# Optimization experiments

Hardware: AMD Instinct MI355X
Metric: run time of the kernel (lower is better)

Reference implementation:

```python
import jax, jax.numpy as jnp
import numpy as np

NEG_INF = -1e9  # stands in for the eye(W)*sys.maxsize self-mask on the row axis


def setup_inputs() -> dict:
    key = jax.random.key(0)
    ks = jax.random.split(key, 8)
    B, C, S = 8, 512, 128
    C8 = C // 8
    sc = 0.02
    x = jax.random.normal(ks[0], (B, C, S, S), dtype=jnp.float32)
    Wq = jax.random.normal(ks[1], (C8, C), dtype=jnp.float32) * sc
    bq = jnp.zeros((C8,), dtype=jnp.float32)
    Wk = jax.random.normal(ks[2], (C8, C), dtype=jnp.float32) * sc
    bk = jnp.zeros((C8,), dtype=jnp.float32)
    Wv = jax.random.normal(ks[3], (C, C), dtype=jnp.float32) * sc
    bv = jnp.zeros((C,), dtype=jnp.float32)
    gamma = jnp.ones((1,), dtype=jnp.float32) * 0.5  # source inits to 0; nonzero so path is exercised
    return {"x": x, "Wq": Wq, "bq": bq, "Wk": Wk, "bk": bk, "Wv": Wv, "bv": bv, "gamma": gamma}


def reference(x, Wq, bq, Wk, bk, Wv, bv, gamma):
    # x: (B, C, W, H) with W == H == S (required by the eye-mask view in the source)
    B, C, S, _ = x.shape
    # 1x1 convs = per-pixel linear projections
    q = jnp.einsum('oc,bcwh->bowh', Wq, x) + bq[None, :, None, None]  # (B,C8,S,S)
    k = jnp.einsum('oc,bcwh->bowh', Wk, x) + bk[None, :, None, None]
    v = jnp.einsum('oc,bcwh->bowh', Wv, x) + bv[None, :, None, None]  # (B,C,S,S)

    # column ('h'-fixed) attention along W, self position masked out
    e_col = jnp.einsum('bcwh,bcuh->bwhu', q, k)  # (B,W,H,W)
    self_mask = jnp.eye(S, dtype=bool)  # w == u
    e_col = jnp.where(self_mask[None, :, None, :], NEG_INF, e_col)
    # row ('w'-fixed) attention along H
    e_row = jnp.einsum('bcwh,bcwu->bwhu', q, k)  # (B,W,H,H)

    att = jax.nn.softmax(jnp.concatenate([e_col, e_row], axis=-1), axis=-1)  # (B,W,H,2S)
    a_col = att[..., :S]   # weights over w'
    a_row = att[..., S:]   # weights over h'

    out = (jnp.einsum('bwhu,bcuh->bcwh', a_col, v)
           + jnp.einsum('bwhu,bcwu->bcwh', a_row, v))  # (B,C,S,S)
    return gamma[0] * out + x
```

## Files before the change

### kernel.cpp

```cpp
#include <hip/hip_runtime.h>
#include <hip/hip_bf16.h>


#define S 128
#define SS 16384
#define C 512
#define C8 64
#define NEG_BIG -1000000000.0f

using short8 = __attribute__((ext_vector_type(8))) short;
using f32x4  = __attribute__((ext_vector_type(4))) float;

#define GPTR(p) ((const __attribute__((address_space(1))) void*)(p))
#define LPTR(p) ((__attribute__((address_space(3))) void*)(p))

#define PR(r) ((((r) & 7) << 4) | ((r) >> 3))

__device__ __forceinline__ unsigned short f2b(float f){
  union { float f; unsigned u; } v; v.f = f;
  unsigned r = (v.u + 0x7fffu + ((v.u >> 16) & 1u)) >> 16;
  return (unsigned short)r;
}
__device__ __forceinline__ float b2f(unsigned short h){
  union { unsigned u; float f; } v; v.u = ((unsigned)h) << 16;
  return v.f;
}

__device__ __forceinline__ void stage_tile64(unsigned short* dst,
    const unsigned short* src, size_t rstride, int tid){
  #pragma unroll
  for (int p = 0; p < 4; ++p){
    int gi = p * 256 + tid;
    int row = gi >> 3, cc = gi & 7;
    int kc = (cc ^ (row & 7)) * 8;
    __builtin_amdgcn_global_load_lds(GPTR(src + (size_t)row * rstride + kc),
                                     LPTR((char*)dst + gi * 16), 16, 0, 0);
  }
}

__global__ __launch_bounds__(256) void k_pack_w(
    const float* __restrict__ Wq, const float* __restrict__ Wk,
    const float* __restrict__ Wv, unsigned short* __restrict__ wall){
  int i = blockIdx.x * 256 + threadIdx.x;
  if (i >= 640 * C) return;
  int co = i >> 9, ci = i & (C - 1);
  float v;
  if (co < 64)        v = Wq[co * C + ci];
  else if (co < 128)  v = Wk[(co - 64) * C + ci];
  else                v = Wv[(co - 128) * C + ci];
  wall[i] = f2b(v);
}

__global__ __launch_bounds__(256) void k_xp(
    const float* __restrict__ x, unsigned short* __restrict__ xp){
  __shared__ unsigned short T[128 * 130] __attribute__((aligned(16)));
  int blk = blockIdx.x;
  int ct = blk & 3; int bw = blk >> 2;
  int w = bw & 127; int b = bw >> 7;
  int tid = threadIdx.x;
  int ci0 = ct * 128;
  const float* xb = x + ((size_t)(b * C + ci0) * S + w) * S;
  #pragma unroll
  for (int p = 0; p < 16; ++p){
    int idx = p * 256 + tid;
    int cc = idx >> 5;
    int h4 = (idx & 31) * 4;
    float4 v = *(const float4*)(xb + (size_t)cc * SS + h4);
    unsigned* d = (unsigned*)&T[PR(cc) * 130 + h4];
    d[0] = (unsigned)f2b(v.x) | ((unsigned)f2b(v.y) << 16);
    d[1] = (unsigned)f2b(v.z) | ((unsigned)f2b(v.w) << 16);
  }
  __syncthreads();
  unsigned short* xpb = xp + (size_t)(b * S + w) * S * C + ci0;
  #pragma unroll
  for (int p = 0; p < 8; ++p){
    int idx = p * 256 + tid;
    int h  = idx >> 4;
    int ch = (idx & 15) * 8;
    unsigned short tmp[8] __attribute__((aligned(16)));
    #pragma unroll
    for (int j = 0; j < 8; ++j) tmp[j] = T[PR(ch + j) * 130 + h];
    *(uint4*)(xpb + (size_t)h * C + ch) = *(uint4*)tmp;
  }
}

__global__ __launch_bounds__(256) void k_qkv(
    const unsigned short* __restrict__ xp, const unsigned short* __restrict__ wall,
    const float* __restrict__ bq, const float* __restrict__ bk,
    const float* __restrict__ bv,
    unsigned short* __restrict__ qp, unsigned short* __restrict__ kp,
    unsigned short* __restrict__ vb){
  __shared__ unsigned short sm[32768] __attribute__((aligned(16)));
  unsigned short* Dl = sm;
  int blk = blockIdx.x;
  int pxsub = blk & 7; int t = blk >> 3;
  int cot = t % 5; int pxg = t / 5;
  int pxt = pxg * 8 + pxsub;
  int w = pxt & 127, b = pxt >> 7;
  int tid = threadIdx.x, lane = tid & 63, wid = tid >> 6;
  int qd = lane >> 4, ln = lane & 15;
  const unsigned short* asrc0 = wall + (size_t)cot * 128 * C;
  const unsigned short* bsrc0 = xp + (size_t)pxt * 128 * C;
  f32x4 acc[4][4];
  #pragma unroll
  for (int i = 0; i < 4; ++i)
    #pragma unroll
    for (int j = 0; j < 4; ++j) acc[i][j] = (f32x4){0.f, 0.f, 0.f, 0.f};

  stage_tile64(sm,        asrc0, C, tid);
  stage_tile64(sm + 8192, bsrc0, C, tid);
  __syncthreads();

  for (int kw = 0; kw < 8; ++kw){
    unsigned short* Acur = sm + (kw & 1) * 16384;
    unsigned short* Bcur = Acur + 8192;
    if (kw < 7){
      unsigned short* Anxt = sm + ((kw + 1) & 1) * 16384;
      stage_tile64(Anxt,        asrc0 + (kw + 1) * 64, C, tid);
      stage_tile64(Anxt + 8192, bsrc0 + (kw + 1) * 64, C, tid);
    }
    __builtin_amdgcn_s_setprio(1);
    #pragma unroll
    for (int ks = 0; ks < 2; ++ks){
      int ch8 = (((ks * 4 + qd) ^ (ln & 7)) * 8);
      short8 af[4], bfr[4];
      #pragma unroll
      for (int i = 0; i < 4; ++i)
        af[i] = *(const short8*)&Acur[(((wid & 1) * 4 + i) * 16 + ln) * 64 + ch8];
      #pragma unroll
      for (int j = 0; j < 4; ++j)
        bfr[j] = *(const short8*)&Bcur[(((wid >> 1) * 4 + j) * 16 + ln) * 64 + ch8];
      #pragma unroll
      for (int i = 0; i < 4; ++i)
        #pragma unroll
        for (int j = 0; j < 4; ++j)
          acc[i][j] = __builtin_amdgcn_mfma_f32_16x16x32_bf16(af[i], bfr[j], acc[i][j], 0, 0, 0);
    }
    __builtin_amdgcn_s_setprio(0);
    __syncthreads();
  }
  float bias_[4][4];
  #pragma unroll
  for (int i = 0; i < 4; ++i){
    int co_l0 = ((wid & 1) * 4 + i) * 16 + qd * 4;
    #pragma unroll
    for (int r = 0; r < 4; ++r){
      int co_l = co_l0 + r;
      bias_[i][r] = (cot == 0) ? (co_l < 64 ? bq[co_l] : bk[co_l - 64])
                               : bv[(cot - 1) * 128 + co_l];
    }
  }
  #pragma unroll
  for (int i = 0; i < 4; ++i){
    int co_l0 = ((wid & 1) * 4 + i) * 16 + qd * 4;
    #pragma unroll
    for (int j = 0; j < 4; ++j){
      int pxl = ((wid >> 1) * 4 + j) * 16 + ln;
      #pragma unroll
      for (int r = 0; r < 4; ++r)
        Dl[(co_l0 + r) * 136 + pxl] = f2b(acc[i][j][r] + bias_[i][r]);
    }
  }
  __syncthreads();
  if (cot == 0){
    unsigned short* qb = qp + (size_t)(b * S + w) * S * C8;
    unsigned short* kb = kp + (size_t)(b * S + w) * S * C8;
    #pragma unroll
    for (int p = 0; p < 4; ++p){
      int idx = p * 256 + tid;
      int cch = idx & 7, hh = idx >> 3;
      unsigned short tq[8] __attribute__((aligned(16)));
      unsigned short tk[8] __attribute__((aligned(16)));
      #pragma unroll
      for (int jj = 0; jj < 8; ++jj){
        tq[jj] = Dl[(cch * 8 + jj) * 136 + hh];
        tk[jj] = Dl[(64 + cch * 8 + jj) * 136 + hh];
      }
      *(uint4*)(qb + (size_t)hh * C8 + cch * 8) = *(uint4*)tq;
      *(uint4*)(kb + (size_t)hh * C8 + cch * 8) = *(uint4*)tk;
    }
  } else {
    unsigned short* vbb = vb + ((size_t)(b * C + (cot - 1) * 128) * S + w) * S;
    #pragma unroll
    for (int p = 0; p < 8; ++p){
      int idx = p * 256 + tid;
      int c_l = idx >> 4, hc = (idx & 15) * 8;
      uint4 v = *(const uint4*)&Dl[c_l * 136 + hc];
      *(uint4*)(vbb + (size_t)c_l * SS + hc) = v;
    }
  }
}

__global__ __launch_bounds__(256) void k_tv(
    const unsigned short* __restrict__ vb, unsigned short* __restrict__ vt){
  __shared__ unsigned short T[128 * 130] __attribute__((aligned(16)));
  int bc = blockIdx.x;
  const unsigned short* src = vb + (size_t)bc * SS;
  unsigned short* dst = vt + (size_t)bc * SS;
  int tid = threadIdx.x;
  #pragma unroll
  for (int p = 0; p < 8; ++p){
    int idx = p * 256 + tid;
    int wv = idx >> 4, ch = (idx & 15) * 8;
    uint4 v = *(const uint4*)(src + wv * S + ch);
    unsigned* d = (unsigned*)&T[PR(wv) * 130 + ch];
    d[0] = v.x; d[1] = v.y; d[2] = v.z; d[3] = v.w;
  }
  __syncthreads();
  #pragma unroll
  for (int p = 0; p < 8; ++p){
    int idx = p * 256 + tid;
    int h = idx >> 4, ch = (idx & 15) * 8;
    unsigned short tmp[8] __attribute__((aligned(16)));
    #pragma unroll
    for (int j = 0; j < 8; ++j) tmp[j] = T[PR(ch + j) * 130 + h];
    *(uint4*)(dst + h * S + ch) = *(uint4*)tmp;
  }
}

__global__ __launch_bounds__(256) void k_ecol(
    const unsigned short* __restrict__ qp, const unsigned short* __restrict__ kp,
    unsigned short* __restrict__ eca){
  __shared__ unsigned short Aq[128 * 72] __attribute__((aligned(16)));
  __shared__ unsigned short Bk[128 * 72] __attribute__((aligned(16)));
  int blk = blockIdx.x; int h = blk & 127, b = blk >> 7;
  int tid = threadIdx.x, lane = tid & 63, wid = tid >> 6;
  int qd = lane >> 4, ln = lane & 15;
  #pragma unroll
  for (int p = 0; p < 4; ++p){
    int idx = p * 256 + tid;
    int row = idx >> 3, ch = (idx & 7) * 8;
    *(uint4*)&Aq[row * 72 + ch] = *(const uint4*)(qp + ((size_t)(b * S + row) * S + h) * C8 + ch);
    *(uint4*)&Bk[row * 72 + ch] = *(const uint4*)(kp + ((size_t)(b * S + row) * S + h) * C8 + ch);
  }
  __syncthreads();
  f32x4 acc[4][4];
  #pragma unroll
  for (int i = 0; i < 4; ++i)
    #pragma unroll
    for (int j = 0; j < 4; ++j) acc[i][j] = (f32x4){0.f, 0.f, 0.f, 0.f};
  #pragma unroll
  for (int ks = 0; ks < 2; ++ks){
    int ko = ks * 32 + qd * 8;
    short8 af[4], bfr[4];
    #pragma unroll
    for (int i = 0; i < 4; ++i)
      af[i] = *(const short8*)&Aq[(((wid & 1) * 4 + i) * 16 + ln) * 72 + ko];
    #pragma unroll
    for (int j = 0; j < 4; ++j)
      bfr[j] = *(const short8*)&Bk[(((wid >> 1) * 4 + j) * 16 + ln) * 72 + ko];
    #pragma unroll
    for (int i = 0; i < 4; ++i)
      #pragma unroll
      for (int j = 0; j < 4; ++j)
        acc[i][j] = __builtin_amdgcn_mfma_f32_16x16x32_bf16(af[i], bfr[j], acc[i][j], 0, 0, 0);
  }
  #pragma unroll
  for (int i = 0; i < 4; ++i){
    int w0 = ((wid & 1) * 4 + i) * 16 + qd * 4;
    #pragma unroll
    for (int j = 0; j < 4; ++j){
      int ug = ((wid >> 1) * 4 + j) * 16 + ln;
      #pragma unroll
      for (int r = 0; r < 4; ++r){
        int wg = w0 + r;
        float val = acc[i][j][r];
        if (wg == ug) val = NEG_BIG;
        eca[((size_t)(b * S + wg) * S + h) * S + ug] = f2b(val);
      }
    }
  }
}

__global__ __launch_bounds__(256) void k_erow_sm_outrow(
    const unsigned short* __restrict__ qp, const unsigned short* __restrict__ kp,
    unsigned short* __restrict__ eca, unsigned short* vb){
  __shared__ char sm[71680] __attribute__((aligned(16)));
  unsigned short* Aq  = (unsigned short*)sm;
  unsigned short* Bk  = (unsigned short*)(sm + 18432);
  unsigned short* El  = (unsigned short*)sm;
  unsigned short* Av0 = (unsigned short*)(sm + 36864);
  unsigned short* Av1 = (unsigned short*)(sm + 53248);
  float* redm = (float*)(sm + 69632);
  float* reds = (float*)(sm + 70656);
  int blk = blockIdx.x; int w = blk & 127, b = blk >> 7;
  int tid = threadIdx.x, lane = tid & 63, wid = tid >> 6;
  int qd = lane >> 4, ln = lane & 15;
  size_t tb = (size_t)(b * S + w) * SS;
  const unsigned short* vsrc0 = vb + (size_t)(b * C) * SS + (size_t)w * S;

  {
    const unsigned short* qsrc = qp + (size_t)(b * S + w) * S * C8;
    const unsigned short* ksrc = kp + (size_t)(b * S + w) * S * C8;
    #pragma unroll
    for (int p = 0; p < 4; ++p){
      int idx = p * 256 + tid;
      int row = idx >> 3, ch = (idx & 7) * 8;
      *(uint4*)&Aq[row * 72 + ch] = *(const uint4*)(qsrc + row * C8 + ch);
      *(uint4*)&Bk[row * 72 + ch] = *(const uint4*)(ksrc + row * C8 + ch);
    }
  }
  stage_tile64(Av0, vsrc0, SS, tid);
  __syncthreads();
  f32x4 acc[4][4];
  #pragma unroll
  for (int i = 0; i < 4; ++i)
    #pragma unroll
    for (int j = 0; j < 4; ++j) acc[i][j] = (f32x4){0.f, 0.f, 0.f, 0.f};
  #pragma unroll
  for (int ks = 0; ks < 2; ++ks){
    int ko = ks * 32 + qd * 8;
    short8 af[4], bfr[4];
    #pragma unroll
    for (int i = 0; i < 4; ++i)
      af[i] = *(const short8*)&Aq[(((wid & 1) * 4 + i) * 16 + ln) * 72 + ko];
    #pragma unroll
    for (int j = 0; j < 4; ++j)
      bfr[j] = *(const short8*)&Bk[(((wid >> 1) * 4 + j) * 16 + ln) * 72 + ko];
    #pragma unroll
    for (int i = 0; i < 4; ++i)
      #pragma unroll
      for (int j = 0; j < 4; ++j)
        acc[i][j] = __builtin_amdgcn_mfma_f32_16x16x32_bf16(af[i], bfr[j], acc[i][j], 0, 0, 0);
  }
  __syncthreads();
  #pragma unroll
  for (int i = 0; i < 4; ++i){
    int h0 = ((wid & 1) * 4 + i) * 16 + qd * 4;
    #pragma unroll
    for (int j = 0; j < 4; ++j){
      int ul = ((wid >> 1) * 4 + j) * 16 + ln;
      #pragma unroll
      for (int r = 0; r < 4; ++r)
        El[(h0 + r) * 136 + ul] = f2b(acc[i][j][r]);
    }
  }
  __syncthreads();
  {
    int h = tid >> 1, half = tid & 1;
    const uint4* src4 = (half == 0) ? (const uint4*)(eca + tb + (size_t)h * S)
                                    : (const uint4*)&El[h * 136];
    float mx = -3.0e38f;
    #pragma unroll 4
    for (int u = 0; u < 16; ++u){
      uint4 v = src4[u];
      const unsigned short* e = (const unsigned short*)&v;
      #pragma unroll
      for (int jj = 0; jj < 8; ++jj) mx = fmaxf(mx, b2f(e[jj]));
    }
    redm[tid] = mx;
    __syncthreads();
    float m = fmaxf(mx, redm[tid ^ 1]);
    float s = 0.f;
    #pragma unroll 4
    for (int u = 0; u < 16; ++u){
      uint4 v = src4[u];
      const unsigned short* e = (const unsigned short*)&v;
      #pragma unroll
      for (int jj = 0; jj < 8; ++jj) s += __expf(b2f(e[jj]) - m);
    }
    reds[tid] = s;
    __syncthreads();
    float inv = 1.0f / (s + reds[tid ^ 1]);
    uint4* dst4 = (half == 0) ? (uint4*)(eca + tb + (size_t)h * S)
                              : (uint4*)&El[h * 136];
    #pragma unroll 4
    for (int u = 0; u < 16; ++u){
      uint4 v = src4[u];
      const unsigned short* e = (const unsigned short*)&v;
      unsigned short o[8] __attribute__((aligned(16)));
      #pragma unroll
      for (int jj = 0; jj < 8; ++jj) o[jj] = f2b(__expf(b2f(e[jj]) - m) * inv);
      dst4[u] = *(uint4*)o;
    }
  }
  __syncthreads();

  for (int s = 0; s < 8; ++s){
    int ct = s >> 1, kw = s & 1;
    unsigned short* Acur = (s & 1) ? Av1 : Av0;
    if (s < 7){
      int ct1 = (s + 1) >> 1, kw1 = (s + 1) & 1;
      stage_tile64((s & 1) ? Av0 : Av1,
                   vsrc0 + (size_t)(ct1 * 128) * SS + kw1 * 64, SS, tid);
    }
    if (kw == 0){
      #pragma unroll
      for (int i = 0; i < 4; ++i)
        #pragma unroll
        for (int j = 0; j < 4; ++j) acc[i][j] = (f32x4){0.f, 0.f, 0.f, 0.f};
    }
    __builtin_amdgcn_s_setprio(1);
    #pragma unroll
    for (int ks = 0; ks < 2; ++ks){
      int ch8 = (((ks * 4 + qd) ^ (ln & 7)) * 8);
      int ko = kw * 64 + ks * 32 + qd * 8;
      short8 af[4], bfr[4];
      #pragma unroll
      for (int i = 0; i < 4; ++i)
        af[i] = *(const short8*)&Acur[(((wid & 1) * 4 + i) * 16 + ln) * 64 + ch8];
      #pragma unroll
      for (int j = 0; j < 4; ++j)
        bfr[j] = *(const short8*)&El[(((wid >> 1) * 4 + j) * 16 + ln) * 136 + ko];
      #pragma unroll
      for (int i = 0; i < 4; ++i)
        #pragma unroll
        for (int j = 0; j < 4; ++j)
          acc[i][j] = __builtin_amdgcn_mfma_f32_16x16x32_bf16(af[i], bfr[j], acc[i][j], 0, 0, 0);
    }
    __builtin_amdgcn_s_setprio(0);
    if (kw == 1){
      #pragma unroll
      for (int i = 0; i < 4; ++i){
        int c0 = ((wid & 1) * 4 + i) * 16 + qd * 4;
        #pragma unroll
        for (int j = 0; j < 4; ++j){
          int hl = ((wid >> 1) * 4 + j) * 16 + ln;
          #pragma unroll
          for (int r = 0; r < 4; ++r){
            int cg = ct * 128 + c0 + r;
            vb[((size_t)(b * C + cg) * S + w) * S + hl] = f2b(acc[i][j][r]);
          }
        }
      }
    }
    __syncthreads();
  }
}

__global__ __launch_bounds__(256) void k_outcol(
    const unsigned short* __restrict__ vt, const unsigned short* __restrict__ eca,
    unsigned short* __restrict__ oct){
  __shared__ unsigned short Av[128 * 72] __attribute__((aligned(16)));
  __shared__ unsigned short Ba[128 * 72] __attribute__((aligned(16)));
  int blk = blockIdx.x;
  int ct = blk & 3; int bh = blk >> 2;
  int h = bh & 127, b = bh >> 7;
  int tid = threadIdx.x, lane = tid & 63, wid = tid >> 6;
  int qd = lane >> 4, ln = lane & 15;
  f32x4 acc[4][4];
  #pragma unroll
  for (int i = 0; i < 4; ++i)
    #pragma unroll
    for (int j = 0; j < 4; ++j) acc[i][j] = (f32x4){0.f, 0.f, 0.f, 0.f};
  for (int kw = 0; kw < 2; ++kw){
    __syncthreads();
    #pragma unroll
    for (int p = 0; p < 4; ++p){
      int idx = p * 256 + tid;
      int row = idx >> 3, ch = (idx & 7) * 8;
      *(uint4*)&Av[row * 72 + ch] =
        *(const uint4*)(vt + ((size_t)(b * C + ct * 128 + row) * S + h) * S + kw * 64 + ch);
      *(uint4*)&Ba[row * 72 + ch] =
        *(const uint4*)(eca + ((size_t)(b * S + row) * S + h) * S + kw * 64 + ch);
    }
    __syncthreads();
    #pragma unroll
    for (int ks = 0; ks < 2; ++ks){
      int ko = ks * 32 + qd * 8;
      short8 af[4], bfr[4];
      #pragma unroll
      for (int i = 0; i < 4; ++i)
        af[i] = *(const short8*)&Av[(((wid & 1) * 4 + i) * 16 + ln) * 72 + ko];
      #pragma unroll
      for (int j = 0; j < 4; ++j)
        bfr[j] = *(const short8*)&Ba[(((wid >> 1) * 4 + j) * 16 + ln) * 72 + ko];
      #pragma unroll
      for (int i = 0; i < 4; ++i)
        #pragma unroll
        for (int j = 0; j < 4; ++j)
          acc[i][j] = __builtin_amdgcn_mfma_f32_16x16x32_bf16(af[i], bfr[j], acc[i][j], 0, 0, 0);
    }
  }
  #pragma unroll
  for (int i = 0; i < 4; ++i){
    int c0 = ((wid & 1) * 4 + i) * 16 + qd * 4;
    #pragma unroll
    for (int j = 0; j < 4; ++j){
      int wl = ((wid >> 1) * 4 + j) * 16 + ln;
      #pragma unroll
      for (int r = 0; r < 4; ++r){
        int cg = ct * 128 + c0 + r;
        oct[((size_t)(b * S + h) * C + cg) * S + wl] = f2b(acc[i][j][r]);
      }
    }
  }
}

__global__ __launch_bounds__(256) void k_final(
    const unsigned short* __restrict__ oct, const unsigned short* __restrict__ orw,
    const float* __restrict__ x, const float* __restrict__ gamma,
    float* __restrict__ out){
  __shared__ unsigned short T[128 * 130] __attribute__((aligned(16)));
  int blk = blockIdx.x;
  int c = blk & 511, b = blk >> 9;
  int tid = threadIdx.x;
  float g = gamma[0];
  #pragma unroll
  for (int p = 0; p < 8; ++p){
    int idx = p * 256 + tid;
    int hh = idx >> 4, ch = (idx & 15) * 8;
    uint4 v = *(const uint4*)(oct + ((size_t)(b * S + hh) * C + c) * S + ch);
    unsigned* d = (unsigned*)&T[PR(hh) * 130 + ch];
    d[0] = v.x; d[1] = v.y; d[2] = v.z; d[3] = v.w;
  }
  __syncthreads();
  #pragma unroll
  for (int p = 0; p < 8; ++p){
    int idx = p * 256 + tid;
    int wv = idx >> 4, hch = (idx & 15) * 8;
    size_t o = ((size_t)(b * C + c) * S + wv) * S + hch;
    uint4 rv = *(const uint4*)(orw + o);
    const unsigned short* rr = (const unsigned short*)&rv;
    float4 x0 = *(const float4*)(x + o);
    float4 x1 = *(const float4*)(x + o + 4);
    float4 o0, o1;
    o0.x = g * (b2f(rr[0]) + b2f(T[PR(hch + 0) * 130 + wv])) + x0.x;
    o0.y = g * (b2f(rr[1]) + b2f(T[PR(hch + 1) * 130 + wv])) + x0.y;
    o0.z = g * (b2f(rr[2]) + b2f(T[PR(hch + 2) * 130 + wv])) + x0.z;
    o0.w = g * (b2f(rr[3]) + b2f(T[PR(hch + 3) * 130 + wv])) + x0.w;
    o1.x = g * (b2f(rr[4]) + b2f(T[PR(hch + 4) * 130 + wv])) + x1.x;
    o1.y = g * (b2f(rr[5]) + b2f(T[PR(hch + 5) * 130 + wv])) + x1.y;
    o1.z = g * (b2f(rr[6]) + b2f(T[PR(hch + 6) * 130 + wv])) + x1.z;
    o1.w = g * (b2f(rr[7]) + b2f(T[PR(hch + 7) * 130 + wv])) + x1.w;
    *(float4*)(out + o) = o0;
    *(float4*)(out + o + 4) = o1;
  }
}

extern "C" void kernel_launch(void* const* d_in, const int* in_sizes, int n_in,
                              void* d_out, int out_size, void* d_ws, size_t ws_size,
                              hipStream_t stream){
  const float* x     = (const float*)d_in[0];
  const float* Wq    = (const float*)d_in[1];
  const float* bq    = (const float*)d_in[2];
  const float* Wk    = (const float*)d_in[3];
  const float* bk    = (const float*)d_in[4];
  const float* Wv    = (const float*)d_in[5];
  const float* bv    = (const float*)d_in[6];
  const float* gamma = (const float*)d_in[7];
  float* out = (float*)d_out;
  char* ws = (char*)d_ws;

  const size_t OFF_WALL = 0;
  const size_t OFF_XP   = 1ull << 20;
  const size_t OFF_QP   = OFF_XP  + 134217728ull;
  const size_t OFF_KP   = OFF_QP  + 16777216ull;
  const size_t OFF_VB   = OFF_KP  + 16777216ull;
  const size_t OFF_VT   = OFF_VB  + 134217728ull;
  const size_t OFF_ECA  = OFF_VT  + 134217728ull;
  const size_t OFF_OCT  = OFF_XP;
  const size_t NEED     = OFF_ECA + 33554432ull;
  if (ws_size < NEED) return;

  unsigned short* wall = (unsigned short*)(ws + OFF_WALL);
  unsigned short* xp   = (unsigned short*)(ws + OFF_XP);
  unsigned short* qp   = (unsigned short*)(ws + OFF_QP);
  unsigned short* kp   = (unsigned short*)(ws + OFF_KP);
  unsigned short* vb   = (unsigned short*)(ws + OFF_VB);
  unsigned short* vt   = (unsigned short*)(ws + OFF_VT);
  unsigned short* eca  = (unsigned short*)(ws + OFF_ECA);
  unsigned short* oct  = (unsigned short*)(ws + OFF_OCT);

  k_pack_w        <<<1280, 256, 0, stream>>>(Wq, Wk, Wv, wall);
  k_xp            <<<4096, 256, 0, stream>>>(x, xp);
  k_qkv           <<<5120, 256, 0, stream>>>(xp, wall, bq, bk, bv, qp, kp, vb);
  k_tv            <<<4096, 256, 0, stream>>>(vb, vt);
  k_ecol          <<<1024, 256, 0, stream>>>(qp, kp, eca);
  k_erow_sm_outrow<<<1024, 256, 0, stream>>>(qp, kp, eca, vb);
  k_outcol        <<<4096, 256, 0, stream>>>(vt, eca, oct);
  k_final         <<<4096, 256, 0, stream>>>(oct, vb, x, gamma, out);
}
```

Before: 921.2 us.

## Merge independent kernels into combined launches and widen QKV GEMM blocks to 8 waves

Weight packing is folded into the x-transpose kernel as extra blocks, and the V transpose is merged with the column-energy kernel in the same way, cutting two kernel launches and the gaps between them. The QKV projection kernel moves from 256 to 512 threads, so each wave computes a 4x2 tile of 16x16 MFMA outputs instead of 4x4, which halves accumulator registers and the per-thread share of LDS staging. The trade-off is that each B fragment loaded from LDS is reused less per wave, and the merged kernels share one LDS allocation sized for the larger branch.

```diff
diff --git a/kernel.cpp b/kernel.cpp
--- a/kernel.cpp
+++ b/kernel.cpp
@@ -26,11 +26,12 @@
   return v.f;
 }
 
+template<int NT>
 __device__ __forceinline__ void stage_tile64(unsigned short* dst,
     const unsigned short* src, size_t rstride, int tid){
   #pragma unroll
-  for (int p = 0; p < 4; ++p){
-    int gi = p * 256 + tid;
+  for (int p = 0; p < 1024 / NT; ++p){
+    int gi = p * NT + tid;
     int row = gi >> 3, cc = gi & 7;
     int kc = (cc ^ (row & 7)) * 8;
     __builtin_amdgcn_global_load_lds(GPTR(src + (size_t)row * rstride + kc),
@@ -38,23 +39,22 @@
   }
 }
 
-__global__ __launch_bounds__(256) void k_pack_w(
+__global__ __launch_bounds__(256) void k_xp_pack(
+    const float* __restrict__ x, unsigned short* __restrict__ xp,
     const float* __restrict__ Wq, const float* __restrict__ Wk,
     const float* __restrict__ Wv, unsigned short* __restrict__ wall){
-  int i = blockIdx.x * 256 + threadIdx.x;
-  if (i >= 640 * C) return;
-  int co = i >> 9, ci = i & (C - 1);
-  float v;
-  if (co < 64)        v = Wq[co * C + ci];
-  else if (co < 128)  v = Wk[(co - 64) * C + ci];
-  else                v = Wv[(co - 128) * C + ci];
-  wall[i] = f2b(v);
-}
-
-__global__ __launch_bounds__(256) void k_xp(
-    const float* __restrict__ x, unsigned short* __restrict__ xp){
   __shared__ unsigned short T[128 * 130] __attribute__((aligned(16)));
   int blk = blockIdx.x;
+  if (blk >= 4096){
+    int i = (blk - 4096) * 256 + threadIdx.x;
+    int co = i >> 9, ci = i & (C - 1);
+    float v;
+    if (co < 64)        v = Wq[co * C + ci];
+    else if (co < 128)  v = Wk[(co - 64) * C + ci];
+    else                v = Wv[(co - 128) * C + ci];
+    wall[i] = f2b(v);
+    return;
+  }
   int ct = blk & 3; int bw = blk >> 2;
   int w = bw & 127; int b = bw >> 7;
   int tid = threadIdx.x;
@@ -84,7 +84,7 @@
   }
 }
 
-__global__ __launch_bounds__(256) void k_qkv(
+__global__ __launch_bounds__(512) void k_qkv(
     const unsigned short* __restrict__ xp, const unsigned short* __restrict__ wall,
     const float* __restrict__ bq, const float* __restrict__ bk,
     const float* __restrict__ bv,
@@ -98,17 +98,18 @@
   int pxt = pxg * 8 + pxsub;
   int w = pxt & 127, b = pxt >> 7;
   int tid = threadIdx.x, lane = tid & 63, wid = tid >> 6;
+  int wr = wid & 1, wc = wid >> 1;
   int qd = lane >> 4, ln = lane & 15;
   const unsigned short* asrc0 = wall + (size_t)cot * 128 * C;
   const unsigned short* bsrc0 = xp + (size_t)pxt * 128 * C;
-  f32x4 acc[4][4];
+  f32x4 acc[4][2];
   #pragma unroll
   for (int i = 0; i < 4; ++i)
     #pragma unroll
-    for (int j = 0; j < 4; ++j) acc[i][j] = (f32x4){0.f, 0.f, 0.f, 0.f};
-
-  stage_tile64(sm,        asrc0, C, tid);
-  stage_tile64(sm + 8192, bsrc0, C, tid);
+    for (int j = 0; j < 2; ++j) acc[i][j] = (f32x4){0.f, 0.f, 0.f, 0.f};
+
+  stage_tile64<512>(sm,        asrc0, C, tid);
+  stage_tile64<512>(sm + 8192, bsrc0, C, tid);
   __syncthreads();
 
   for (int kw = 0; kw < 8; ++kw){
@@ -116,24 +117,24 @@
     unsigned short* Bcur = Acur + 8192;
     if (kw < 7){
       unsigned short* Anxt = sm + ((kw + 1) & 1) * 16384;
-      stage_tile64(Anxt,        asrc0 + (kw + 1) * 64, C, tid);
-      stage_tile64(Anxt + 8192, bsrc0 + (kw + 1) * 64, C, tid);
+      stage_tile64<512>(Anxt,        asrc0 + (kw + 1) * 64, C, tid);
+      stage_tile64<512>(Anxt + 8192, bsrc0 + (kw + 1) * 64, C, tid);
     }
     __builtin_amdgcn_s_setprio(1);
     #pragma unroll
     for (int ks = 0; ks < 2; ++ks){
       int ch8 = (((ks * 4 + qd) ^ (ln & 7)) * 8);
-      short8 af[4], bfr[4];
-      #pragma unroll
-      for (int i = 0; i < 4; ++i)
-        af[i] = *(const short8*)&Acur[(((wid & 1) * 4 + i) * 16 + ln) * 64 + ch8];
-      #pragma unroll
-      for (int j = 0; j < 4; ++j)
-        bfr[j] = *(const short8*)&Bcur[(((wid >> 1) * 4 + j) * 16 + ln) * 64 + ch8];
+      short8 af[4], bfr[2];
+      #pragma unroll
+      for (int i = 0; i < 4; ++i)
+        af[i] = *(const short8*)&Acur[((wr * 4 + i) * 16 + ln) * 64 + ch8];
+      #pragma unroll
+      for (int j = 0; j < 2; ++j)
+        bfr[j] = *(const short8*)&Bcur[((wc * 2 + j) * 16 + ln) * 64 + ch8];
       #pragma unroll
       for (int i = 0; i < 4; ++i)
         #pragma unroll
-        for (int j = 0; j < 4; ++j)
+        for (int j = 0; j < 2; ++j)
           acc[i][j] = __builtin_amdgcn_mfma_f32_16x16x32_bf16(af[i], bfr[j], acc[i][j], 0, 0, 0);
     }
     __builtin_amdgcn_s_setprio(0);
@@ -142,7 +143,7 @@
   float bias_[4][4];
   #pragma unroll
   for (int i = 0; i < 4; ++i){
-    int co_l0 = ((wid & 1) * 4 + i) * 16 + qd * 4;
+    int co_l0 = (wr * 4 + i) * 16 + qd * 4;
     #pragma unroll
     for (int r = 0; r < 4; ++r){
       int co_l = co_l0 + r;
@@ -152,10 +153,10 @@
   }
   #pragma unroll
   for (int i = 0; i < 4; ++i){
-    int co_l0 = ((wid & 1) * 4 + i) * 16 + qd * 4;
-    #pragma unroll
-    for (int j = 0; j < 4; ++j){
-      int pxl = ((wid >> 1) * 4 + j) * 16 + ln;
+    int co_l0 = (wr * 4 + i) * 16 + qd * 4;
+    #pragma unroll
+    for (int j = 0; j < 2; ++j){
+      int pxl = (wc * 2 + j) * 16 + ln;
       #pragma unroll
       for (int r = 0; r < 4; ++r)
         Dl[(co_l0 + r) * 136 + pxl] = f2b(acc[i][j][r] + bias_[i][r]);
@@ -166,8 +167,8 @@
     unsigned short* qb = qp + (size_t)(b * S + w) * S * C8;
     unsigned short* kb = kp + (size_t)(b * S + w) * S * C8;
     #pragma unroll
-    for (int p = 0; p < 4; ++p){
-      int idx = p * 256 + tid;
+    for (int p = 0; p < 2; ++p){
+      int idx = p * 512 + tid;
       int cch = idx & 7, hh = idx >> 3;
       unsigned short tq[8] __attribute__((aligned(16)));
       unsigned short tk[8] __attribute__((aligned(16)));
@@ -182,8 +183,8 @@
   } else {
     unsigned short* vbb = vb + ((size_t)(b * C + (cot - 1) * 128) * S + w) * S;
     #pragma unroll
-    for (int p = 0; p < 8; ++p){
-      int idx = p * 256 + tid;
+    for (int p = 0; p < 4; ++p){
+      int idx = p * 512 + tid;
       int c_l = idx >> 4, hc = (idx & 15) * 8;
       uint4 v = *(const uint4*)&Dl[c_l * 136 + hc];
       *(uint4*)(vbb + (size_t)c_l * SS + hc) = v;
@@ -191,40 +192,41 @@
   }
 }
 
-__global__ __launch_bounds__(256) void k_tv(
-    const unsigned short* __restrict__ vb, unsigned short* __restrict__ vt){
-  __shared__ unsigned short T[128 * 130] __attribute__((aligned(16)));
-  int bc = blockIdx.x;
-  const unsigned short* src = vb + (size_t)bc * SS;
-  unsigned short* dst = vt + (size_t)bc * SS;
-  int tid = threadIdx.x;
-  #pragma unroll
-  for (int p = 0; p < 8; ++p){
-    int idx = p * 256 + tid;
-    int wv = idx >> 4, ch = (idx & 15) * 8;
-    uint4 v = *(const uint4*)(src + wv * S + ch);
-    unsigned* d = (unsigned*)&T[PR(wv) * 130 + ch];
-    d[0] = v.x; d[1] = v.y; d[2] = v.z; d[3] = v.w;
-  }
-  __syncthreads();
-  #pragma unroll
-  for (int p = 0; p < 8; ++p){
-    int idx = p * 256 + tid;
-    int h = idx >> 4, ch = (idx & 15) * 8;
-    unsigned short tmp[8] __attribute__((aligned(16)));
-    #pragma unroll
-    for (int j = 0; j < 8; ++j) tmp[j] = T[PR(ch + j) * 130 + h];
-    *(uint4*)(dst + h * S + ch) = *(uint4*)tmp;
-  }
-}
-
-__global__ __launch_bounds__(256) void k_ecol(
+__global__ __launch_bounds__(256) void k_tv_ecol(
+    const unsigned short* __restrict__ vb, unsigned short* __restrict__ vt,
     const unsigned short* __restrict__ qp, const unsigned short* __restrict__ kp,
     unsigned short* __restrict__ eca){
-  __shared__ unsigned short Aq[128 * 72] __attribute__((aligned(16)));
-  __shared__ unsigned short Bk[128 * 72] __attribute__((aligned(16)));
-  int blk = blockIdx.x; int h = blk & 127, b = blk >> 7;
-  int tid = threadIdx.x, lane = tid & 63, wid = tid >> 6;
+  __shared__ char smu[36864] __attribute__((aligned(16)));
+  int blk = blockIdx.x;
+  int tid = threadIdx.x;
+  if (blk < 4096){
+    unsigned short* T = (unsigned short*)smu;
+    const unsigned short* src = vb + (size_t)blk * SS;
+    unsigned short* dst = vt + (size_t)blk * SS;
+    #pragma unroll
+    for (int p = 0; p < 8; ++p){
+      int idx = p * 256 + tid;
+      int wv = idx >> 4, ch = (idx & 15) * 8;
+      uint4 v = *(const uint4*)(src + wv * S + ch);
+      unsigned* d = (unsigned*)&T[PR(wv) * 130 + ch];
+      d[0] = v.x; d[1] = v.y; d[2] = v.z; d[3] = v.w;
+    }
+    __syncthreads();
+    #pragma unroll
+    for (int p = 0; p < 8; ++p){
+      int idx = p * 256 + tid;
+      int h = idx >> 4, ch = (idx & 15) * 8;
+      unsigned short tmp[8] __attribute__((aligned(16)));
+      #pragma unroll
+      for (int j = 0; j < 8; ++j) tmp[j] = T[PR(ch + j) * 130 + h];
+      *(uint4*)(dst + h * S + ch) = *(uint4*)tmp;
+    }
+    return;
+  }
+  unsigned short* Aq = (unsigned short*)smu;
+  unsigned short* Bk = (unsigned short*)(smu + 18432);
+  int e = blk - 4096; int h = e & 127, b = e >> 7;
+  int lane = tid & 63, wid = tid >> 6;
   int qd = lane >> 4, ln = lane & 15;
   #pragma unroll
   for (int p = 0; p < 4; ++p){
@@ -257,7 +259,7 @@
   }
   #pragma unroll
   for (int i = 0; i < 4; ++i){
-    int w0 = ((wid & 1) * 4 + i) * 16 + qd * 4;
+    int w0 = (((wid & 1) * 4 + i) * 16) + qd * 4;
     #pragma unroll
     for (int j = 0; j < 4; ++j){
       int ug = ((wid >> 1) * 4 + j) * 16 + ln;
@@ -300,7 +302,7 @@
       *(uint4*)&Bk[row * 72 + ch] = *(const uint4*)(ksrc + row * C8 + ch);
     }
   }
-  stage_tile64(Av0, vsrc0, SS, tid);
+  stage_tile64<256>(Av0, vsrc0, SS, tid);
   __syncthreads();
   f32x4 acc[4][4];
   #pragma unroll
@@ -381,8 +383,8 @@
     unsigned short* Acur = (s & 1) ? Av1 : Av0;
     if (s < 7){
       int ct1 = (s + 1) >> 1, kw1 = (s + 1) & 1;
-      stage_tile64((s & 1) ? Av0 : Av1,
-                   vsrc0 + (size_t)(ct1 * 128) * SS + kw1 * 64, SS, tid);
+      stage_tile64<256>((s & 1) ? Av0 : Av1,
+                        vsrc0 + (size_t)(ct1 * 128) * SS + kw1 * 64, SS, tid);
     }
     if (kw == 0){
       #pragma unroll
@@ -562,11 +564,9 @@
   unsigned short* eca  = (unsigned short*)(ws + OFF_ECA);
   unsigned short* oct  = (unsigned short*)(ws + OFF_OCT);
 
-  k_pack_w        <<<1280, 256, 0, stream>>>(Wq, Wk, Wv, wall);
-  k_xp            <<<4096, 256, 0, stream>>>(x, xp);
-  k_qkv           <<<5120, 256, 0, stream>>>(xp, wall, bq, bk, bv, qp, kp, vb);
-  k_tv            <<<4096, 256, 0, stream>>>(vb, vt);
-  k_ecol          <<<1024, 256, 0, stream>>>(qp, kp, eca);
+  k_xp_pack       <<<5376, 256, 0, stream>>>(x, xp, Wq, Wk, Wv, wall);
+  k_qkv           <<<5120, 512, 0, stream>>>(xp, wall, bq, bk, bv, qp, kp, vb);
+  k_tv_ecol       <<<5120, 256, 0, stream>>>(vb, vt, qp, kp, eca);
   k_erow_sm_outrow<<<1024, 256, 0, stream>>>(qp, kp, eca, vb);
   k_outcol        <<<4096, 256, 0, stream>>>(vt, eca, oct);
   k_final         <<<4096, 256, 0, stream>>>(oct, vb, x, gamma, out);
```

Measured after the change: 917.3 us. About the same (-0.4%).
